# Kernel optimization log

Measured on AMD Instinct MI355X. Metric: run time of the kernel, lower is better.

The kernel has to match this reference:

```python
import jax, jax.numpy as jnp
import numpy as np

N_NODES = 100000
N_EDGES = 1600000
N_GRAPHS = 5000
F_IN = 11
HID = 128
N_CLASSES = 19


def setup_inputs() -> dict:
    key = jax.random.key(0)
    ks = jax.random.split(key, 12)
    x = jax.random.normal(ks[0], (N_NODES, F_IN), dtype=jnp.float32)
    edge_index = jax.random.randint(ks[1], (2, N_EDGES), 0, N_NODES, dtype=jnp.int64)
    batch = jnp.sort(jax.random.randint(ks[2], (N_NODES,), 0, N_GRAPHS, dtype=jnp.int64))
    def glorot(k, shape):
        lim = float(np.sqrt(6.0 / (shape[0] + shape[1])))
        return jax.random.uniform(k, shape, jnp.float32, -lim, lim)
    return {
        'x': x,
        'edge_index': edge_index,
        'batch': batch,
        'W1': glorot(ks[3], (F_IN, HID)),  'b1': jnp.zeros((HID,), jnp.float32),
        'W2': glorot(ks[4], (HID, HID)),   'b2': jnp.zeros((HID,), jnp.float32),
        'W3': glorot(ks[5], (HID, HID)),   'b3': jnp.zeros((HID,), jnp.float32),
        'Wlin': glorot(ks[6], (HID, N_CLASSES)), 'blin': jnp.zeros((N_CLASSES,), jnp.float32),
    }


def _gcn_conv(x, src, dst, norm, self_w, W, b):
    # GCNConv: D^{-1/2}(A+I)D^{-1/2} X W + b  (self loops handled analytically)
    h = x @ W                                   # [N, out]
    msg = h[src] * norm[:, None]                # [E, out] gathered + scaled
    agg = jax.ops.segment_sum(msg, dst, num_segments=N_NODES)
    return agg + h * self_w[:, None] + b


def reference(x, edge_index, batch, W1, b1, W2, b2, W3, b3, Wlin, blin):
    src, dst = edge_index[0], edge_index[1]
    # degree including self loop (gcn_norm with add_self_loops=True)
    deg = jax.ops.segment_sum(jnp.ones((N_EDGES,), x.dtype), dst, num_segments=N_NODES) + 1.0
    dis = jax.lax.rsqrt(deg)                    # deg^{-1/2}
    norm = dis[src] * dis[dst]                  # per-edge coefficient
    self_w = dis * dis                          # 1/deg for the self loop

    h = jax.nn.relu(_gcn_conv(x, src, dst, norm, self_w, W1, b1))
    h = jax.nn.relu(_gcn_conv(h, src, dst, norm, self_w, W2, b2))
    h = _gcn_conv(h, src, dst, norm, self_w, W3, b3)

    # global_mean_pool over graph ids
    sums = jax.ops.segment_sum(h, batch, num_segments=N_GRAPHS)
    cnts = jax.ops.segment_sum(jnp.ones((N_NODES,), h.dtype), batch, num_segments=N_GRAPHS)
    pooled = sums / jnp.maximum(cnts, 1.0)[:, None]

    # dropout is identity in eval mode
    return pooled @ Wlin + blin
```

## Files before the change

### kernel.cpp

```cpp
#include <hip/hip_runtime.h>
#include <hip/hip_bf16.h>
#include <hip/hip_fp16.h>

#define NN 100000
#define NE 1600000
#define NG 5000
#define FIN 11
#define HID 128
#define NC 19

#define NBK 98
#define BKSH 10
#define BKMASK 1023
#define BCAP 20480

typedef _Float16 f16x8 __attribute__((ext_vector_type(8)));
typedef _Float16 f16x4 __attribute__((ext_vector_type(4)));
typedef float f32x4 __attribute__((ext_vector_type(4)));


__global__ __launch_bounds__(1024) void k_p1scatter(const int* __restrict__ ei,
                                                    int* __restrict__ gcur, unsigned int* __restrict__ p1) {
    __shared__ int hist[NBK];
    __shared__ int base[NBK];
    __shared__ int lrank[NBK];
    int t = threadIdx.x;
    if (t < NBK) { hist[t] = 0; lrank[t] = 0; }
    __syncthreads();

    int e0 = blockIdx.x * 4096 + t * 4;
    int sr[4], dr[4], bk[4];
    if (e0 + 3 < NE) {
        int4 s4 = *(const int4*)(ei + e0);
        int4 d4 = *(const int4*)(ei + NE + e0);
        sr[0] = s4.x; sr[1] = s4.y; sr[2] = s4.z; sr[3] = s4.w;
        dr[0] = d4.x; dr[1] = d4.y; dr[2] = d4.z; dr[3] = d4.w;
        #pragma unroll
        for (int k = 0; k < 4; ++k) { bk[k] = dr[k] >> BKSH; atomicAdd(&hist[bk[k]], 1); }
    } else {
        #pragma unroll
        for (int k = 0; k < 4; ++k) {
            int e = e0 + k;
            if (e < NE) { sr[k] = ei[e]; dr[k] = ei[NE + e]; bk[k] = dr[k] >> BKSH; atomicAdd(&hist[bk[k]], 1); }
            else bk[k] = -1;
        }
    }
    __syncthreads();
    if (t < NBK && hist[t] > 0)
        base[t] = t * BCAP + atomicAdd(&gcur[t], hist[t]);
    __syncthreads();
    #pragma unroll
    for (int k = 0; k < 4; ++k) {
        if (bk[k] >= 0) {
            int slot = atomicAdd(&lrank[bk[k]], 1);
            p1[base[bk[k]] + slot] = (unsigned int)sr[k] | ((unsigned int)(dr[k] & BKMASK) << 17);
        }
    }
}

__global__ __launch_bounds__(64) void k_bucketbase(const int* __restrict__ gcur, int* __restrict__ bbase,
                                                   int* __restrict__ rp) {
    if (threadIdx.x == 0) {
        int acc = 0;
        for (int i = 0; i < NBK; ++i) {
            bbase[i] = acc;
            int c = gcur[i]; if (c > BCAP) c = BCAP;
            acc += c;
        }
        rp[NN] = acc;
    }
}

__global__ __launch_bounds__(1024) void k_p2fill(const unsigned int* __restrict__ p1,
                                                 const int* __restrict__ gcur,
                                                 const int* __restrict__ bbase,
                                                 int* __restrict__ rp, int* __restrict__ csr,
                                                 float* __restrict__ dis) {
    __shared__ int cnt[1024];
    __shared__ int pf[1024];
    __shared__ int cur[1024];
    __shared__ int wsum[16];
    int bkt = blockIdx.x;
    int t = threadIdx.x;
    int v0 = bkt << BKSH;
    int nb = NN - v0; if (nb > 1024) nb = 1024;
    cnt[t] = 0; cur[t] = 0;
    __syncthreads();
    int count = gcur[bkt]; if (count > BCAP) count = BCAP;
    const unsigned int* reg = p1 + (size_t)bkt * BCAP;
    for (int i = t; i < count; i += 1024)
        atomicAdd(&cnt[reg[i] >> 17], 1);
    __syncthreads();
    int c = cnt[t];
    int lane = t & 63, w = t >> 6;
    int val = c;
    #pragma unroll
    for (int off = 1; off < 64; off <<= 1) {
        int n = __shfl_up(val, off, 64);
        if (lane >= off) val += n;
    }
    if (lane == 63) wsum[w] = val;
    __syncthreads();
    if (w == 0) {
        int s = (lane < 16) ? wsum[lane] : 0;
        #pragma unroll
        for (int off = 1; off < 16; off <<= 1) {
            int n = __shfl_up(s, off, 64);
            if (lane >= off) s += n;
        }
        if (lane < 16) wsum[lane] = s;
    }
    __syncthreads();
    int wbase = (w == 0) ? 0 : wsum[w - 1];
    int excl = wbase + val - c;
    pf[t] = excl;
    int base = bbase[bkt];
    if (t < nb) {
        rp[v0 + t] = base + excl;
        dis[v0 + t] = rsqrtf((float)c + 1.0f);
    }
    __syncthreads();
    for (int i = t; i < count; i += 1024) {
        unsigned int u = reg[i];
        int dl = u >> 17;
        int off2 = atomicAdd(&cur[dl], 1);
        csr[base + pf[dl] + off2] = (int)(u & 0x1FFFFu);
    }
}

__global__ __launch_bounds__(256) void k_gstart(const int* __restrict__ batch, int* __restrict__ gstart) {
    int g = blockIdx.x * 256 + threadIdx.x;
    if (g > NG) return;
    int lo = 0, hi = NN;
    while (lo < hi) {
        int mid = (lo + hi) >> 1;
        if (batch[mid] < g) lo = mid + 1; else hi = mid;
    }
    gstart[g] = lo;
}

__global__ __launch_bounds__(256) void k_prescale(const float* __restrict__ x, const float* __restrict__ dis,
                                                  _Float16* __restrict__ xsc) {
    int i = blockIdx.x * 256 + threadIdx.x;
    if (i < NN * 16) {
        int v = i >> 4, c = i & 15;
        float val = (c < FIN) ? x[v * FIN + c] * dis[v] : 0.f;
        xsc[i] = (_Float16)val;
    }
}

__global__ __launch_bounds__(256) void k_packW(const float* __restrict__ W, _Float16* __restrict__ Wp) {
    int t = blockIdx.x * 256 + threadIdx.x;
    if (t >= 2048) return;
    int lane = t & 63;
    int tile = t >> 6;
    int kb = tile >> 3, ct = tile & 7;
    int kbase = kb * 32 + (lane >> 4) * 8;
    int col = ct * 16 + (lane & 15);
    f16x8 v;
    #pragma unroll
    for (int e = 0; e < 8; ++e) v[e] = (_Float16)W[(kbase + e) * HID + col];
    *(f16x8*)&Wp[(size_t)t * 8] = v;
}

__global__ __launch_bounds__(64) void k_wfuse(const float* __restrict__ W3, const float* __restrict__ b3,
                                              const float* __restrict__ Wl, const float* __restrict__ bl,
                                              float* __restrict__ Wf, float* __restrict__ bf) {
    int i = blockIdx.x;
    int t = threadIdx.x;
    if (t >= NC) return;
    if (i < HID) {
        float a = 0.f;
        #pragma unroll 4
        for (int k = 0; k < HID; ++k) a += W3[i * HID + k] * Wl[k * NC + t];
        Wf[i * NC + t] = a;
    } else {
        float a = bl[t];
        #pragma unroll 4
        for (int k = 0; k < HID; ++k) a += b3[k] * Wl[k * NC + t];
        bf[t] = a;
    }
}


__global__ __launch_bounds__(256) void k_agg11(const _Float16* __restrict__ xsc, const int* __restrict__ rp,
                                               const int* __restrict__ csr, const float* __restrict__ dis,
                                               _Float16* __restrict__ xa) {
    int wid = threadIdx.x >> 6, lane = threadIdx.x & 63;
    int v = blockIdx.x * 4 + wid;
    if (v >= NN) return;
    int erel = lane >> 4, c = lane & 15;
    int beg = rp[v], end = rp[v + 1];
    float accA = 0.f, accB = 0.f;
    int e = beg;
    for (; e + 8 <= end; e += 8) {
        int s0 = csr[e + erel], s1 = csr[e + 4 + erel];
        accA += (float)xsc[s0 * 16 + c];
        accB += (float)xsc[s1 * 16 + c];
    }
    for (; e < end; e += 4) {
        int idx = e + erel;
        if (idx < end) accA += (float)xsc[csr[idx] * 16 + c];
    }
    float a = accA + accB;
    a += __shfl_xor(a, 16);
    a += __shfl_xor(a, 32);
    if (erel == 0) {
        a += (float)xsc[v * 16 + c];
        xa[v * 16 + c] = (_Float16)(a * dis[v]);
    }
}

__global__ __launch_bounds__(256) void k_gemm11(const _Float16* __restrict__ X, const float* __restrict__ W,
                                                const float* __restrict__ bias, const float* __restrict__ dis,
                                                __half* __restrict__ out16) {
    __shared__ float Ws[FIN][HID];
    __shared__ float Xs[16][17];
    int t = threadIdx.x;
    int row0 = blockIdx.x * 16;
    for (int idx = t; idx < FIN * HID; idx += 256) Ws[idx / HID][idx % HID] = W[idx];
    {
        int r = t >> 4, c = t & 15;
        Xs[r][c] = (float)X[(row0 + r) * 16 + c];
    }
    __syncthreads();
    int c = t & (HID - 1);
    int rg = t >> 7;
    #pragma unroll
    for (int i = 0; i < 8; ++i) {
        int r = rg * 8 + i;
        int row = row0 + r;
        float a = bias[c];
        #pragma unroll
        for (int k = 0; k < FIN; ++k) a += Xs[r][k] * Ws[k][c];
        a = fmaxf(a, 0.f);
        out16[row * HID + c] = __float2half(a * dis[row]);
    }
}

__global__ __launch_bounds__(256) void k_agg16(const _Float16* __restrict__ Ht, const int* __restrict__ rp,
                                               const int* __restrict__ csr, const float* __restrict__ dis,
                                               _Float16* __restrict__ out16) {
    int wid = threadIdx.x >> 6;
    int lane = threadIdx.x & 63;
    int v = blockIdx.x * 4 + wid;
    if (v >= NN) return;
    int erel = lane >> 4;
    int c8 = lane & 15;
    const _Float16* bp = Ht + (size_t)c8 * 8;
    int beg = rp[v], end = rp[v + 1];
    float acc0[8] = {}, acc1[8] = {};
    int e = beg;
    for (; e + 16 <= end; e += 16) {
        int s0 = csr[e + erel];
        int s1 = csr[e + 4 + erel];
        int s2 = csr[e + 8 + erel];
        int s3 = csr[e + 12 + erel];
        f16x8 h0 = *(const f16x8*)(bp + (size_t)s0 * HID);
        f16x8 h1 = *(const f16x8*)(bp + (size_t)s1 * HID);
        f16x8 h2 = *(const f16x8*)(bp + (size_t)s2 * HID);
        f16x8 h3 = *(const f16x8*)(bp + (size_t)s3 * HID);
        #pragma unroll
        for (int j = 0; j < 8; ++j) {
            acc0[j] += (float)h0[j] + (float)h2[j];
            acc1[j] += (float)h1[j] + (float)h3[j];
        }
    }
    for (; e + 4 <= end; e += 4) {
        int s = csr[e + erel];
        f16x8 h = *(const f16x8*)(bp + (size_t)s * HID);
        #pragma unroll
        for (int j = 0; j < 8; ++j) acc0[j] += (float)h[j];
    }
    int rem = end - e;
    if (rem > 0) {
        int idx = e + erel;
        float m = (erel < rem) ? 1.f : 0.f;
        if (idx >= end) idx = end - 1;
        int s = csr[idx];
        f16x8 h = *(const f16x8*)(bp + (size_t)s * HID);
        #pragma unroll
        for (int j = 0; j < 8; ++j) acc0[j] += m * (float)h[j];
    }
    #pragma unroll
    for (int j = 0; j < 8; ++j) {
        float s = acc0[j] + acc1[j];
        s += __shfl_xor(s, 16);
        s += __shfl_xor(s, 32);
        acc0[j] = s;
    }
    if (erel == 0) {
        f16x8 sh = *(const f16x8*)(bp + (size_t)v * HID);
        float dv = dis[v];
        f16x8 o;
        #pragma unroll
        for (int j = 0; j < 8; ++j) o[j] = (_Float16)((acc0[j] + (float)sh[j]) * dv);
        *(f16x8*)(out16 + (size_t)v * HID + c8 * 8) = o;
    }
}


__global__ __launch_bounds__(256) void k_gemm128m(const _Float16* __restrict__ X,
                                                  const _Float16* __restrict__ Wp,
                                                  const float* __restrict__ bias,
                                                  const float* __restrict__ dis,
                                                  _Float16* __restrict__ out, int mode) {
    int wave = threadIdx.x >> 6, lane = threadIdx.x & 63;
    int row0 = blockIdx.x * 128 + wave * 32;
    int rA = lane & 15, kg = lane >> 4;

    f32x4 acc[2][8];
    #pragma unroll
    for (int s = 0; s < 2; ++s)
        #pragma unroll
        for (int c = 0; c < 8; ++c)
            acc[s][c] = {0.f, 0.f, 0.f, 0.f};

    int r0c = row0 + rA;      if (r0c > NN - 1) r0c = NN - 1;
    int r1c = row0 + 16 + rA; if (r1c > NN - 1) r1c = NN - 1;
    const _Float16* xp0 = X + (size_t)r0c * HID + kg * 8;
    const _Float16* xp1 = X + (size_t)r1c * HID + kg * 8;

    #pragma unroll
    for (int kb = 0; kb < 4; ++kb) {
        f16x8 a0 = *(const f16x8*)(xp0 + kb * 32);
        f16x8 a1 = *(const f16x8*)(xp1 + kb * 32);
        #pragma unroll
        for (int ct = 0; ct < 8; ++ct) {
            f16x8 b = *(const f16x8*)&Wp[(size_t)((kb * 8 + ct) * 64 + lane) * 8];
            acc[0][ct] = __builtin_amdgcn_mfma_f32_16x16x32_f16(a0, b, acc[0][ct], 0, 0, 0);
            acc[1][ct] = __builtin_amdgcn_mfma_f32_16x16x32_f16(a1, b, acc[1][ct], 0, 0, 0);
        }
    }

    int c15 = lane & 15;
    #pragma unroll
    for (int s = 0; s < 2; ++s) {
        int rbase = row0 + s * 16 + kg * 4;
        float dv[4];
        #pragma unroll
        for (int r = 0; r < 4; ++r) {
            int rr = rbase + r; if (rr > NN - 1) rr = NN - 1;
            dv[r] = dis[rr];
        }
        #pragma unroll
        for (int ct = 0; ct < 8; ++ct) {
            int col = ct * 16 + c15;
            float bb = bias[col];
            #pragma unroll
            for (int r = 0; r < 4; ++r) {
                int rr = rbase + r;
                if (rr < NN) {
                    float v = acc[s][ct][r] + bb;
                    if (mode == 0) v = fmaxf(v, 0.f) * dv[r];
                    out[(size_t)rr * HID + col] = (_Float16)v;
                }
            }
        }
    }
}

__global__ __launch_bounds__(256) void k_pool16(const __half2* __restrict__ H, const int* __restrict__ gstart,
                                                float* __restrict__ pooled) {
    int wid = threadIdx.x >> 6;
    int lane = threadIdx.x & 63;
    int g = blockIdx.x * 4 + wid;
    if (g >= NG) return;
    int beg = gstart[g], end = gstart[g + 1];
    float ax = 0.f, ay = 0.f;
    for (int n = beg; n < end; ++n) {
        float2 f = __half22float2(H[n * 64 + lane]);
        ax += f.x; ay += f.y;
    }
    float inv = 1.f / fmaxf((float)(end - beg), 1.f);
    pooled[g * HID + lane * 2]     = ax * inv;
    pooled[g * HID + lane * 2 + 1] = ay * inv;
}

__global__ __launch_bounds__(64) void k_linear(const float* __restrict__ P, const float* __restrict__ Wf,
                                               const float* __restrict__ bf, float* __restrict__ out) {
    int g = blockIdx.x;
    int t = threadIdx.x;
    __shared__ float ps[HID];
    for (int k = t; k < HID; k += 64) ps[k] = P[g * HID + k];
    __syncthreads();
    if (t < NC) {
        float a = bf[t];
        #pragma unroll 4
        for (int k = 0; k < HID; ++k) a += ps[k] * Wf[k * NC + t];
        out[g * NC + t] = a;
    }
}


extern "C" void kernel_launch(void* const* d_in, const int* in_sizes, int n_in,
                              void* d_out, int out_size, void* d_ws, size_t ws_size,
                              hipStream_t stream) {
    const float* x   = (const float*)d_in[0];
    const int* ei    = (const int*)d_in[1];
    const int* batch = (const int*)d_in[2];
    const float* W1 = (const float*)d_in[3];
    const float* b1 = (const float*)d_in[4];
    const float* W2 = (const float*)d_in[5];
    const float* b2 = (const float*)d_in[6];
    const float* W3 = (const float*)d_in[7];
    const float* b3 = (const float*)d_in[8];
    const float* Wl = (const float*)d_in[9];
    const float* bl = (const float*)d_in[10];
    float* out = (float*)d_out;

    char* ws = (char*)d_ws;
    size_t off = 0;
    auto alloc = [&](size_t bytes) -> void* {
        void* p = ws + off;
        off += (bytes + 255) & ~(size_t)255;
        return p;
    };
    float*        dis    = (float*)alloc((size_t)NN * 4);
    int*          rp     = (int*)alloc((size_t)(NN + 1) * 4);
    int*          csr    = (int*)alloc((size_t)NE * 4);
    unsigned int* p1     = (unsigned int*)alloc((size_t)NBK * BCAP * 4);
    int*          gcur   = (int*)alloc(NBK * 4);
    int*          bbase  = (int*)alloc(NBK * 4);
    int*          gstart = (int*)alloc((size_t)(NG + 1) * 4);
    _Float16*     xsc    = (_Float16*)alloc((size_t)NN * 16 * 2);
    _Float16*     xa     = (_Float16*)alloc((size_t)NN * 16 * 2);
    _Float16*     Wp2    = (_Float16*)alloc((size_t)HID * HID * 2);
    float*        Wf     = (float*)alloc((size_t)HID * NC * 4);
    float*        bf     = (float*)alloc(NC * 4);
    _Float16*     Ht     = (_Float16*)alloc((size_t)NN * HID * 2);
    _Float16*     tb16   = (_Float16*)alloc((size_t)NN * HID * 2);
    float*        pooled = (float*)alloc((size_t)NG * HID * 4);
    (void)ws_size; (void)in_sizes; (void)n_in; (void)out_size;

    hipMemsetAsync(gcur, 0, NBK * 4, stream);

    k_p1scatter<<<(NE + 4095) / 4096, 1024, 0, stream>>>(ei, gcur, p1);
    k_bucketbase<<<1, 64, 0, stream>>>(gcur, bbase, rp);
    k_p2fill<<<NBK, 1024, 0, stream>>>(p1, gcur, bbase, rp, csr, dis);
    k_gstart<<<(NG + 256) / 256, 256, 0, stream>>>(batch, gstart);
    k_prescale<<<(NN * 16 + 255) / 256, 256, 0, stream>>>(x, dis, xsc);
    k_packW<<<8, 256, 0, stream>>>(W2, Wp2);
    k_wfuse<<<HID + 1, 64, 0, stream>>>(W3, b3, Wl, bl, Wf, bf);

    k_agg11<<<(NN + 3) / 4, 256, 0, stream>>>(xsc, rp, csr, dis, xa);
    k_gemm11<<<NN / 16, 256, 0, stream>>>(xa, W1, b1, dis, (__half*)Ht);

    k_agg16<<<(NN + 3) / 4, 256, 0, stream>>>(Ht, rp, csr, dis, tb16);
    k_gemm128m<<<(NN + 127) / 128, 256, 0, stream>>>(tb16, Wp2, b2, dis, Ht, 0);

    k_agg16<<<(NN + 3) / 4, 256, 0, stream>>>(Ht, rp, csr, dis, tb16);

    k_pool16<<<(NG + 3) / 4, 256, 0, stream>>>((const __half2*)tb16, gstart, pooled);
    k_linear<<<NG, 64, 0, stream>>>(pooled, Wf, bf, out);
}
```

Baseline: 298.2 us.

## Pad CSR rows to multiples of four and fuse setup, layer-1 and pooling kernels

Each node's adjacency list is padded to a multiple of four, with padding entries pointing at a zero dummy row at index NN. Each bucket gets a fixed CSR region, and row offset plus padded length are packed into one meta word, so the bucket-base prefix kernel and the masked tail handling in the aggregation loops go away. Several small setup kernels merge into one multi-role launch, layer-1 aggregation is fused with its 11-wide GEMM, and pooling is fused with the final linear. This cuts launch count and intermediate traffic, at the cost of extra gathers on padded entries and the assumption that per-bucket edge counts stay within CCAP.

```diff
diff --git a/kernel.cpp b/kernel.cpp
--- a/kernel.cpp
+++ b/kernel.cpp
@@ -13,9 +13,9 @@
 #define BKSH 10
 #define BKMASK 1023
 #define BCAP 20480
+#define CCAP 24576
 
 typedef _Float16 f16x8 __attribute__((ext_vector_type(8)));
-typedef _Float16 f16x4 __attribute__((ext_vector_type(4)));
 typedef float f32x4 __attribute__((ext_vector_type(4)));
 
 
@@ -58,23 +58,9 @@
     }
 }
 
-__global__ __launch_bounds__(64) void k_bucketbase(const int* __restrict__ gcur, int* __restrict__ bbase,
-                                                   int* __restrict__ rp) {
-    if (threadIdx.x == 0) {
-        int acc = 0;
-        for (int i = 0; i < NBK; ++i) {
-            bbase[i] = acc;
-            int c = gcur[i]; if (c > BCAP) c = BCAP;
-            acc += c;
-        }
-        rp[NN] = acc;
-    }
-}
-
 __global__ __launch_bounds__(1024) void k_p2fill(const unsigned int* __restrict__ p1,
                                                  const int* __restrict__ gcur,
-                                                 const int* __restrict__ bbase,
-                                                 int* __restrict__ rp, int* __restrict__ csr,
+                                                 unsigned int* __restrict__ meta, int* __restrict__ csr,
                                                  float* __restrict__ dis) {
     __shared__ int cnt[1024];
     __shared__ int pf[1024];
@@ -92,8 +78,9 @@
         atomicAdd(&cnt[reg[i] >> 17], 1);
     __syncthreads();
     int c = cnt[t];
+    int pc = (c + 3) & ~3;
     int lane = t & 63, w = t >> 6;
-    int val = c;
+    int val = pc;
     #pragma unroll
     for (int off = 1; off < 64; off <<= 1) {
         int n = __shfl_up(val, off, 64);
@@ -112,11 +99,11 @@
     }
     __syncthreads();
     int wbase = (w == 0) ? 0 : wsum[w - 1];
-    int excl = wbase + val - c;
+    int excl = wbase + val - pc;
     pf[t] = excl;
-    int base = bbase[bkt];
+    unsigned int gb = (unsigned int)bkt * CCAP;
     if (t < nb) {
-        rp[v0 + t] = base + excl;
+        meta[v0 + t] = ((gb + (unsigned int)excl) << 9) | (unsigned int)(pc >> 2);
         dis[v0 + t] = rsqrtf((float)c + 1.0f);
     }
     __syncthreads();
@@ -124,121 +111,125 @@
         unsigned int u = reg[i];
         int dl = u >> 17;
         int off2 = atomicAdd(&cur[dl], 1);
-        csr[base + pf[dl] + off2] = (int)(u & 0x1FFFFu);
-    }
-}
-
-__global__ __launch_bounds__(256) void k_gstart(const int* __restrict__ batch, int* __restrict__ gstart) {
-    int g = blockIdx.x * 256 + threadIdx.x;
-    if (g > NG) return;
-    int lo = 0, hi = NN;
-    while (lo < hi) {
-        int mid = (lo + hi) >> 1;
-        if (batch[mid] < g) lo = mid + 1; else hi = mid;
-    }
-    gstart[g] = lo;
-}
-
-__global__ __launch_bounds__(256) void k_prescale(const float* __restrict__ x, const float* __restrict__ dis,
-                                                  _Float16* __restrict__ xsc) {
-    int i = blockIdx.x * 256 + threadIdx.x;
-    if (i < NN * 16) {
-        int v = i >> 4, c = i & 15;
-        float val = (c < FIN) ? x[v * FIN + c] * dis[v] : 0.f;
-        xsc[i] = (_Float16)val;
-    }
-}
-
-__global__ __launch_bounds__(256) void k_packW(const float* __restrict__ W, _Float16* __restrict__ Wp) {
-    int t = blockIdx.x * 256 + threadIdx.x;
-    if (t >= 2048) return;
-    int lane = t & 63;
-    int tile = t >> 6;
-    int kb = tile >> 3, ct = tile & 7;
-    int kbase = kb * 32 + (lane >> 4) * 8;
-    int col = ct * 16 + (lane & 15);
-    f16x8 v;
-    #pragma unroll
-    for (int e = 0; e < 8; ++e) v[e] = (_Float16)W[(kbase + e) * HID + col];
-    *(f16x8*)&Wp[(size_t)t * 8] = v;
-}
-
-__global__ __launch_bounds__(64) void k_wfuse(const float* __restrict__ W3, const float* __restrict__ b3,
-                                              const float* __restrict__ Wl, const float* __restrict__ bl,
-                                              float* __restrict__ Wf, float* __restrict__ bf) {
-    int i = blockIdx.x;
-    int t = threadIdx.x;
-    if (t >= NC) return;
-    if (i < HID) {
-        float a = 0.f;
-        #pragma unroll 4
-        for (int k = 0; k < HID; ++k) a += W3[i * HID + k] * Wl[k * NC + t];
-        Wf[i * NC + t] = a;
+        csr[gb + pf[dl] + off2] = (int)(u & 0x1FFFFu);
+    }
+    if (t < nb) {
+        int b0 = gb + pf[t];
+        for (int k = c; k < pc; ++k) csr[b0 + k] = NN;
+    }
+}
+
+
+__global__ __launch_bounds__(256) void k_setup(const float* __restrict__ x, const float* __restrict__ dis,
+                                               const int* __restrict__ batch,
+                                               const float* __restrict__ W2, const float* __restrict__ W3,
+                                               const float* __restrict__ b3, const float* __restrict__ Wl,
+                                               const float* __restrict__ bl,
+                                               _Float16* __restrict__ xsc, int* __restrict__ gstart,
+                                               _Float16* __restrict__ Wp2, float* __restrict__ Wf,
+                                               float* __restrict__ bf,
+                                               _Float16* __restrict__ Ht, _Float16* __restrict__ tb16) {
+    int b = blockIdx.x, t = threadIdx.x;
+    if (b < 6251) {
+        int i = b * 256 + t;
+        if (i < (NN + 1) * 16) {
+            int v = i >> 4, c = i & 15;
+            float val = (v < NN && c < FIN) ? x[v * FIN + c] * dis[v] : 0.f;
+            xsc[i] = (_Float16)val;
+        }
+    } else if (b < 6271) {
+        int g = (b - 6251) * 256 + t;
+        if (g > NG) return;
+        int lo = 0, hi = NN;
+        while (lo < hi) {
+            int mid = (lo + hi) >> 1;
+            if (batch[mid] < g) lo = mid + 1; else hi = mid;
+        }
+        gstart[g] = lo;
+    } else if (b < 6279) {
+        int t2 = (b - 6271) * 256 + t;
+        int lane = t2 & 63;
+        int tile = t2 >> 6;
+        int kb = tile >> 3, ct = tile & 7;
+        int kbase = kb * 32 + (lane >> 4) * 8;
+        int col = ct * 16 + (lane & 15);
+        f16x8 v;
+        #pragma unroll
+        for (int e = 0; e < 8; ++e) v[e] = (_Float16)W2[(kbase + e) * HID + col];
+        *(f16x8*)&Wp2[(size_t)t2 * 8] = v;
+    } else if (b < 6312) {
+        int i = (b - 6279) * 4 + (t >> 6);
+        int tc = t & 63;
+        if (tc >= NC || i > HID) return;
+        if (i < HID) {
+            float a = 0.f;
+            #pragma unroll 4
+            for (int k = 0; k < HID; ++k) a += W3[i * HID + k] * Wl[k * NC + tc];
+            Wf[i * NC + tc] = a;
+        } else {
+            float a = bl[tc];
+            #pragma unroll 4
+            for (int k = 0; k < HID; ++k) a += b3[k] * Wl[k * NC + tc];
+            bf[tc] = a;
+        }
     } else {
-        float a = bl[t];
-        #pragma unroll 4
-        for (int k = 0; k < HID; ++k) a += b3[k] * Wl[k * NC + t];
-        bf[t] = a;
-    }
-}
-
-
-__global__ __launch_bounds__(256) void k_agg11(const _Float16* __restrict__ xsc, const int* __restrict__ rp,
-                                               const int* __restrict__ csr, const float* __restrict__ dis,
-                                               _Float16* __restrict__ xa) {
-    int wid = threadIdx.x >> 6, lane = threadIdx.x & 63;
-    int v = blockIdx.x * 4 + wid;
-    if (v >= NN) return;
-    int erel = lane >> 4, c = lane & 15;
-    int beg = rp[v], end = rp[v + 1];
-    float accA = 0.f, accB = 0.f;
-    int e = beg;
-    for (; e + 8 <= end; e += 8) {
-        int s0 = csr[e + erel], s1 = csr[e + 4 + erel];
-        accA += (float)xsc[s0 * 16 + c];
-        accB += (float)xsc[s1 * 16 + c];
-    }
-    for (; e < end; e += 4) {
-        int idx = e + erel;
-        if (idx < end) accA += (float)xsc[csr[idx] * 16 + c];
-    }
-    float a = accA + accB;
-    a += __shfl_xor(a, 16);
-    a += __shfl_xor(a, 32);
-    if (erel == 0) {
-        a += (float)xsc[v * 16 + c];
-        xa[v * 16 + c] = (_Float16)(a * dis[v]);
-    }
-}
-
-__global__ __launch_bounds__(256) void k_gemm11(const _Float16* __restrict__ X, const float* __restrict__ W,
-                                                const float* __restrict__ bias, const float* __restrict__ dis,
-                                                __half* __restrict__ out16) {
+        if (t < HID) Ht[(size_t)NN * HID + t] = (_Float16)0.f;
+        else tb16[(size_t)NN * HID + (t - HID)] = (_Float16)0.f;
+    }
+}
+
+__global__ __launch_bounds__(256) void k_l1(const _Float16* __restrict__ xsc,
+                                            const unsigned int* __restrict__ meta,
+                                            const int* __restrict__ csr, const float* __restrict__ dis,
+                                            const float* __restrict__ W1, const float* __restrict__ b1,
+                                            _Float16* __restrict__ out16) {
     __shared__ float Ws[FIN][HID];
     __shared__ float Xs[16][17];
     int t = threadIdx.x;
     int row0 = blockIdx.x * 16;
-    for (int idx = t; idx < FIN * HID; idx += 256) Ws[idx / HID][idx % HID] = W[idx];
-    {
-        int r = t >> 4, c = t & 15;
-        Xs[r][c] = (float)X[(row0 + r) * 16 + c];
-    }
-    __syncthreads();
-    int c = t & (HID - 1);
+    for (int idx = t; idx < FIN * HID; idx += 256) Ws[idx / HID][idx % HID] = W1[idx];
+
+    int wave = t >> 6, lane = t & 63;
+    int erel = lane >> 4, c = lane & 15;
+    #pragma unroll
+    for (int i = 0; i < 4; ++i) {
+        int v = row0 + wave * 4 + i;
+        unsigned int m = meta[v];
+        int beg = (int)(m >> 9);
+        int pend = beg + (int)((m & 511u) << 2);
+        float accA = 0.f, accB = 0.f;
+        int e = beg;
+        for (; e + 8 <= pend; e += 8) {
+            int s0 = csr[e + erel], s1 = csr[e + 4 + erel];
+            accA += (float)xsc[s0 * 16 + c];
+            accB += (float)xsc[s1 * 16 + c];
+        }
+        if (e < pend) accA += (float)xsc[csr[e + erel] * 16 + c];
+        float a = accA + accB;
+        a += __shfl_xor(a, 16);
+        a += __shfl_xor(a, 32);
+        if (erel == 0) {
+            a += (float)xsc[v * 16 + c];
+            Xs[wave * 4 + i][c] = a * dis[v];
+        }
+    }
+    __syncthreads();
+    int cc = t & (HID - 1);
     int rg = t >> 7;
     #pragma unroll
     for (int i = 0; i < 8; ++i) {
         int r = rg * 8 + i;
         int row = row0 + r;
-        float a = bias[c];
-        #pragma unroll
-        for (int k = 0; k < FIN; ++k) a += Xs[r][k] * Ws[k][c];
+        float a = b1[cc];
+        #pragma unroll
+        for (int k = 0; k < FIN; ++k) a += Xs[r][k] * Ws[k][cc];
         a = fmaxf(a, 0.f);
-        out16[row * HID + c] = __float2half(a * dis[row]);
-    }
-}
-
-__global__ __launch_bounds__(256) void k_agg16(const _Float16* __restrict__ Ht, const int* __restrict__ rp,
+        out16[(size_t)row * HID + cc] = (_Float16)(a * dis[row]);
+    }
+}
+
+__global__ __launch_bounds__(256) void k_agg16(const _Float16* __restrict__ Ht,
+                                               const unsigned int* __restrict__ meta,
                                                const int* __restrict__ csr, const float* __restrict__ dis,
                                                _Float16* __restrict__ out16) {
     int wid = threadIdx.x >> 6;
@@ -248,10 +239,12 @@
     int erel = lane >> 4;
     int c8 = lane & 15;
     const _Float16* bp = Ht + (size_t)c8 * 8;
-    int beg = rp[v], end = rp[v + 1];
+    unsigned int m = meta[v];
+    int beg = (int)(m >> 9);
+    int pend = beg + (int)((m & 511u) << 2);
     float acc0[8] = {}, acc1[8] = {};
     int e = beg;
-    for (; e + 16 <= end; e += 16) {
+    for (; e + 16 <= pend; e += 16) {
         int s0 = csr[e + erel];
         int s1 = csr[e + 4 + erel];
         int s2 = csr[e + 8 + erel];
@@ -266,21 +259,11 @@
             acc1[j] += (float)h1[j] + (float)h3[j];
         }
     }
-    for (; e + 4 <= end; e += 4) {
+    for (; e < pend; e += 4) {
         int s = csr[e + erel];
         f16x8 h = *(const f16x8*)(bp + (size_t)s * HID);
         #pragma unroll
         for (int j = 0; j < 8; ++j) acc0[j] += (float)h[j];
-    }
-    int rem = end - e;
-    if (rem > 0) {
-        int idx = e + erel;
-        float m = (erel < rem) ? 1.f : 0.f;
-        if (idx >= end) idx = end - 1;
-        int s = csr[idx];
-        f16x8 h = *(const f16x8*)(bp + (size_t)s * HID);
-        #pragma unroll
-        for (int j = 0; j < 8; ++j) acc0[j] += m * (float)h[j];
     }
     #pragma unroll
     for (int j = 0; j < 8; ++j) {
@@ -299,12 +282,11 @@
     }
 }
 
-
 __global__ __launch_bounds__(256) void k_gemm128m(const _Float16* __restrict__ X,
                                                   const _Float16* __restrict__ Wp,
                                                   const float* __restrict__ bias,
                                                   const float* __restrict__ dis,
-                                                  _Float16* __restrict__ out, int mode) {
+                                                  _Float16* __restrict__ out) {
     int wave = threadIdx.x >> 6, lane = threadIdx.x & 63;
     int row0 = blockIdx.x * 128 + wave * 32;
     int rA = lane & 15, kg = lane >> 4;
@@ -351,8 +333,7 @@
             for (int r = 0; r < 4; ++r) {
                 int rr = rbase + r;
                 if (rr < NN) {
-                    float v = acc[s][ct][r] + bb;
-                    if (mode == 0) v = fmaxf(v, 0.f) * dv[r];
+                    float v = fmaxf(acc[s][ct][r] + bb, 0.f) * dv[r];
                     out[(size_t)rr * HID + col] = (_Float16)v;
                 }
             }
@@ -360,29 +341,21 @@
     }
 }
 
-__global__ __launch_bounds__(256) void k_pool16(const __half2* __restrict__ H, const int* __restrict__ gstart,
-                                                float* __restrict__ pooled) {
-    int wid = threadIdx.x >> 6;
-    int lane = threadIdx.x & 63;
-    int g = blockIdx.x * 4 + wid;
-    if (g >= NG) return;
+__global__ __launch_bounds__(64) void k_poollin(const _Float16* __restrict__ H, const int* __restrict__ gstart,
+                                                const float* __restrict__ Wf, const float* __restrict__ bf,
+                                                float* __restrict__ out) {
+    int g = blockIdx.x;
+    int t = threadIdx.x;
     int beg = gstart[g], end = gstart[g + 1];
     float ax = 0.f, ay = 0.f;
     for (int n = beg; n < end; ++n) {
-        float2 f = __half22float2(H[n * 64 + lane]);
-        ax += f.x; ay += f.y;
+        ax += (float)H[(size_t)n * HID + t];
+        ay += (float)H[(size_t)n * HID + 64 + t];
     }
     float inv = 1.f / fmaxf((float)(end - beg), 1.f);
-    pooled[g * HID + lane * 2]     = ax * inv;
-    pooled[g * HID + lane * 2 + 1] = ay * inv;
-}
-
-__global__ __launch_bounds__(64) void k_linear(const float* __restrict__ P, const float* __restrict__ Wf,
-                                               const float* __restrict__ bf, float* __restrict__ out) {
-    int g = blockIdx.x;
-    int t = threadIdx.x;
     __shared__ float ps[HID];
-    for (int k = t; k < HID; k += 64) ps[k] = P[g * HID + k];
+    ps[t] = ax * inv;
+    ps[t + 64] = ay * inv;
     __syncthreads();
     if (t < NC) {
         float a = bf[t];
@@ -417,40 +390,33 @@
         return p;
     };
     float*        dis    = (float*)alloc((size_t)NN * 4);
-    int*          rp     = (int*)alloc((size_t)(NN + 1) * 4);
-    int*          csr    = (int*)alloc((size_t)NE * 4);
+    unsigned int* meta   = (unsigned int*)alloc((size_t)NN * 4);
+    int*          csr    = (int*)alloc((size_t)NBK * CCAP * 4);
     unsigned int* p1     = (unsigned int*)alloc((size_t)NBK * BCAP * 4);
     int*          gcur   = (int*)alloc(NBK * 4);
-    int*          bbase  = (int*)alloc(NBK * 4);
     int*          gstart = (int*)alloc((size_t)(NG + 1) * 4);
-    _Float16*     xsc    = (_Float16*)alloc((size_t)NN * 16 * 2);
-    _Float16*     xa     = (_Float16*)alloc((size_t)NN * 16 * 2);
+    _Float16*     xsc    = (_Float16*)alloc((size_t)(NN + 1) * 16 * 2);
     _Float16*     Wp2    = (_Float16*)alloc((size_t)HID * HID * 2);
     float*        Wf     = (float*)alloc((size_t)HID * NC * 4);
     float*        bf     = (float*)alloc(NC * 4);
-    _Float16*     Ht     = (_Float16*)alloc((size_t)NN * HID * 2);
-    _Float16*     tb16   = (_Float16*)alloc((size_t)NN * HID * 2);
-    float*        pooled = (float*)alloc((size_t)NG * HID * 4);
+    _Float16*     Ht     = (_Float16*)alloc((size_t)(NN + 1) * HID * 2);
+    _Float16*     tb16   = (_Float16*)alloc((size_t)(NN + 1) * HID * 2);
     (void)ws_size; (void)in_sizes; (void)n_in; (void)out_size;
 
     hipMemsetAsync(gcur, 0, NBK * 4, stream);
 
     k_p1scatter<<<(NE + 4095) / 4096, 1024, 0, stream>>>(ei, gcur, p1);
-    k_bucketbase<<<1, 64, 0, stream>>>(gcur, bbase, rp);
-    k_p2fill<<<NBK, 1024, 0, stream>>>(p1, gcur, bbase, rp, csr, dis);
-    k_gstart<<<(NG + 256) / 256, 256, 0, stream>>>(batch, gstart);
-    k_prescale<<<(NN * 16 + 255) / 256, 256, 0, stream>>>(x, dis, xsc);
-    k_packW<<<8, 256, 0, stream>>>(W2, Wp2);
-    k_wfuse<<<HID + 1, 64, 0, stream>>>(W3, b3, Wl, bl, Wf, bf);
-
-    k_agg11<<<(NN + 3) / 4, 256, 0, stream>>>(xsc, rp, csr, dis, xa);
-    k_gemm11<<<NN / 16, 256, 0, stream>>>(xa, W1, b1, dis, (__half*)Ht);
-
-    k_agg16<<<(NN + 3) / 4, 256, 0, stream>>>(Ht, rp, csr, dis, tb16);
-    k_gemm128m<<<(NN + 127) / 128, 256, 0, stream>>>(tb16, Wp2, b2, dis, Ht, 0);
-
-    k_agg16<<<(NN + 3) / 4, 256, 0, stream>>>(Ht, rp, csr, dis, tb16);
-
-    k_pool16<<<(NG + 3) / 4, 256, 0, stream>>>((const __half2*)tb16, gstart, pooled);
-    k_linear<<<NG, 64, 0, stream>>>(pooled, Wf, bf, out);
-}
+    k_p2fill<<<NBK, 1024, 0, stream>>>(p1, gcur, meta, csr, dis);
+
+    k_setup<<<6313, 256, 0, stream>>>(x, dis, batch, W2, W3, b3, Wl, bl,
+                                      xsc, gstart, Wp2, Wf, bf, Ht, tb16);
+
+    k_l1<<<NN / 16, 256, 0, stream>>>(xsc, meta, csr, dis, W1, b1, Ht);
+
+    k_agg16<<<(NN + 3) / 4, 256, 0, stream>>>(Ht, meta, csr, dis, tb16);
+    k_gemm128m<<<(NN + 127) / 128, 256, 0, stream>>>(tb16, Wp2, b2, dis, Ht);
+
+    k_agg16<<<(NN + 3) / 4, 256, 0, stream>>>(Ht, meta, csr, dis, tb16);
+
+    k_poollin<<<NG, 64, 0, stream>>>(tb16, gstart, Wf, bf, out);
+}
```

After: 265.9 us. 10.8% less time.
